# Kernel optimization log

Hardware: AMD Instinct MI355X
Metric: run time of the kernel (lower is better)

The kernel has to match this reference:

```python
import jax, jax.numpy as jnp
import numpy as np

N_NODES = 100000
N_EDGES = 1600000
F_IN = 128
HID = 128
N_CLS = 10
BN_EPS = 1e-5


def setup_inputs() -> dict:
    key = jax.random.key(0)
    ks = jax.random.split(key, 20)
    d = {}
    d['x'] = jax.random.normal(ks[0], (N_NODES, F_IN), dtype=jnp.float32)
    d['edge_index'] = jax.random.randint(ks[1], (2, N_EDGES), 0, N_NODES, dtype=jnp.int64)
    d['edge_weights'] = jax.random.uniform(ks[2], (N_EDGES,), dtype=jnp.float32)
    s1 = 1.0 / np.sqrt(F_IN)
    s2 = 1.0 / np.sqrt(HID)
    d['W1'] = jax.random.normal(ks[3], (F_IN, HID), dtype=jnp.float32) * s1
    d['b1'] = jax.random.normal(ks[4], (HID,), dtype=jnp.float32) * 0.01
    d['g1'] = jax.random.uniform(ks[5], (HID,), dtype=jnp.float32) + 0.5
    d['be1'] = jax.random.normal(ks[6], (HID,), dtype=jnp.float32) * 0.01
    d['W2'] = jax.random.normal(ks[7], (HID, HID), dtype=jnp.float32) * s2
    d['b2'] = jax.random.normal(ks[8], (HID,), dtype=jnp.float32) * 0.01
    d['g2'] = jax.random.uniform(ks[9], (HID,), dtype=jnp.float32) + 0.5
    d['be2'] = jax.random.normal(ks[10], (HID,), dtype=jnp.float32) * 0.01
    d['W3'] = jax.random.normal(ks[11], (HID, HID), dtype=jnp.float32) * s2
    d['b3'] = jax.random.normal(ks[12], (HID,), dtype=jnp.float32) * 0.01
    d['g3'] = jax.random.uniform(ks[13], (HID,), dtype=jnp.float32) + 0.5
    d['be3'] = jax.random.normal(ks[14], (HID,), dtype=jnp.float32) * 0.01
    d['Wlin'] = jax.random.normal(ks[15], (3 * HID, N_CLS), dtype=jnp.float32) / np.sqrt(3 * HID)
    d['blin'] = jax.random.normal(ks[16], (N_CLS,), dtype=jnp.float32) * 0.01
    return d


def _gcn_norm(edge_index, edge_weights, n):
    # add self loops with weight 1 (PyG gcn_norm default fill_value=1)
    loops = jnp.arange(n, dtype=edge_index.dtype)
    row = jnp.concatenate([edge_index[0], loops])   # source j
    col = jnp.concatenate([edge_index[1], loops])   # target i
    ew = jnp.concatenate([edge_weights, jnp.ones((n,), edge_weights.dtype)])
    deg = jax.ops.segment_sum(ew, col, num_segments=n)  # in-degree by weight
    dis = jnp.where(deg > 0, jax.lax.rsqrt(deg), 0.0)
    norm = dis[row] * ew * dis[col]                     # [E+N]
    return row, col, norm


def _gcn_conv(x, row, col, norm, W, b, n):
    h = x @ W                                            # [N, H]
    msg = h[row] * norm[:, None]                         # gather + scale
    out = jax.ops.segment_sum(msg, col, num_segments=n)  # scatter-add
    return out + b


def _bn_relu(x, g, be):
    # BatchNorm with track_running_stats=False: batch stats, biased variance
    mean = jnp.mean(x, axis=0)
    var = jnp.mean((x - mean) ** 2, axis=0)
    y = (x - mean) * jax.lax.rsqrt(var + BN_EPS) * g + be
    return jax.nn.relu(y)


def reference(x, edge_index, edge_weights, W1, b1, g1, be1, W2, b2, g2, be2,
              W3, b3, g3, be3, Wlin, blin):
    n = x.shape[0]
    row, col, norm = _gcn_norm(edge_index, edge_weights, n)
    o1 = _bn_relu(_gcn_conv(x, row, col, norm, W1, b1, n), g1, be1)
    o2 = _bn_relu(_gcn_conv(o1, row, col, norm, W2, b2, n), g2, be2)
    o3 = _bn_relu(_gcn_conv(o2, row, col, norm, W3, b3, n), g3, be3)
    emb = jnp.concatenate([o1, o2, o3], axis=1)          # [N, 3H]
    return emb @ Wlin + blin                             # [N, C]
```

## Files before the change

### kernel.cpp

```cpp
#include <hip/hip_runtime.h>

#define BN_EPS 1e-5f
#define AGG_GRID 2048
#define RED1 64
#define NB 512
#define CAP 4864
#define BIN_KE 16

typedef __attribute__((ext_vector_type(8))) short short8;
typedef __attribute__((ext_vector_type(4))) float f32x4;

static __device__ __forceinline__ float4 ld4(const float* p){ return *reinterpret_cast<const float4*>(p); }
static __device__ __forceinline__ void st4(float* p, float4 v){ *reinterpret_cast<float4*>(p) = v; }
static __device__ __forceinline__ unsigned short f2bf(float f){
  unsigned u = __float_as_uint(f);
  u += 0x7fffu + ((u>>16)&1u);
  return (unsigned short)(u>>16);
}
static __device__ __forceinline__ void fma_bf4(float4& a, float s, uint2 w){
  float v0 = __uint_as_float(w.x << 16);
  float v1 = __uint_as_float(w.x & 0xffff0000u);
  float v2 = __uint_as_float(w.y << 16);
  float v3 = __uint_as_float(w.y & 0xffff0000u);
  a.x = fmaf(s,v0,a.x); a.y = fmaf(s,v1,a.y); a.z = fmaf(s,v2,a.z); a.w = fmaf(s,v3,a.w);
}

__global__ __launch_bounds__(256) void k_zero(int* p, int n){
  int i = blockIdx.x*256 + threadIdx.x;
  if (i < n) p[i] = 0;
}

__global__ __launch_bounds__(256) void k_prepW(const float* __restrict__ W, unsigned short* __restrict__ Wt){
  int idx = blockIdx.x*256 + threadIdx.x;
  int k = idx >> 7, n = idx & 127;
  Wt[n*128 + k] = f2bf(W[idx]);
}

__global__ __launch_bounds__(256) void k_bin(const int* __restrict__ row, const int* __restrict__ col,
                                             const float* __restrict__ ew, int* __restrict__ bucketCnt,
                                             int2* __restrict__ bin, int E){
  __shared__ int hist[NB];
  int t = threadIdx.x;
  hist[t] = 0; hist[t+256] = 0;
  __syncthreads();
  int base0 = blockIdx.x*(256*BIN_KE) + t;
  int rank[BIN_KE];
  #pragma unroll
  for (int j=0;j<BIN_KE;++j){
    int e = base0 + j*256;
    if (e < E) rank[j] = atomicAdd(&hist[col[e]>>8], 1);
  }
  __syncthreads();
  int c0 = hist[t], c1 = hist[t+256];
  __syncthreads();
  if (c0) hist[t]     = atomicAdd(&bucketCnt[t],     c0);
  if (c1) hist[t+256] = atomicAdd(&bucketCnt[t+256], c1);
  __syncthreads();
  #pragma unroll
  for (int j=0;j<BIN_KE;++j){
    int e = base0 + j*256;
    if (e < E){
      int d = col[e];
      int bk = d >> 8;
      int pos = hist[bk] + rank[j];
      if (pos < CAP)
        bin[(size_t)bk*CAP + pos] = make_int2(row[e] | ((d & 255) << 17), __float_as_int(ew[e]));
    }
  }
}

__global__ void k_scan512(const int* __restrict__ cnt, int* __restrict__ start){
  __shared__ int sh[NB];
  int t = threadIdx.x;
  int c = cnt[t]; if (c > CAP) c = CAP;
  sh[t] = c;
  __syncthreads();
  for (int off=1; off<NB; off<<=1){
    int x = (t>=off) ? sh[t-off] : 0;
    __syncthreads();
    sh[t] += x;
    __syncthreads();
  }
  start[t] = sh[t] - c;
}

__global__ __launch_bounds__(256) void k_csr(const int2* __restrict__ bin, const int* __restrict__ bucketCnt,
                                             const int* __restrict__ bucketStart, int2* __restrict__ csr,
                                             int* __restrict__ rstart, float* __restrict__ deg, int N){
  __shared__ int hist[256], scn[256];
  __shared__ float degl[256];
  int b = blockIdx.x, t = threadIdx.x;
  hist[t] = 0; degl[t] = 0.f;
  __syncthreads();
  int m = bucketCnt[b]; if (m > CAP) m = CAP;
  const int2* bb = bin + (size_t)b*CAP;
  for (int i = t; i < m; i += 256){
    int2 r = bb[i];
    int dl = (r.x >> 17) & 255;
    atomicAdd(&hist[dl], 1);
    atomicAdd(&degl[dl], __int_as_float(r.y));
  }
  __syncthreads();
  int c = hist[t];
  scn[t] = c;
  __syncthreads();
  for (int off=1; off<256; off<<=1){
    int x = (t>=off) ? scn[t-off] : 0;
    __syncthreads();
    scn[t] += x;
    __syncthreads();
  }
  int base = bucketStart[b];
  int g = (b<<8) + t;
  if (g < N){
    rstart[g] = base + scn[t] - c;
    deg[g] = 1.f + degl[t];
    if (g == N-1) rstart[N] = base + scn[t];
  }
  __syncthreads();
  hist[t] = scn[t] - c;
  __syncthreads();
  for (int i = t; i < m; i += 256){
    int2 r = bb[i];
    int dl = (r.x >> 17) & 255;
    int pos = atomicAdd(&hist[dl], 1);
    csr[base + pos] = make_int2(r.x & 0x1FFFF, r.y);
  }
}

__global__ __launch_bounds__(256) void k_dis(const float* __restrict__ deg, float* __restrict__ dis, int N){
  int i = blockIdx.x*256 + threadIdx.x;
  if (i < N) dis[i] = rsqrtf(deg[i]);
}

__global__ __launch_bounds__(256) void k_norm(int2* __restrict__ csr, const float* __restrict__ dis, int M){
  int e = blockIdx.x*256 + threadIdx.x;
  if (e < M){
    int2 r = csr[e];
    r.y = __float_as_int(__int_as_float(r.y) * dis[r.x]);
    csr[e] = r;
  }
}

template<bool BN>
__global__ __launch_bounds__(256) void k_gemm_mfma(const float* __restrict__ A, const unsigned short* __restrict__ Wt,
                                                   const float* __restrict__ abv, unsigned short* __restrict__ h, int N){
  __shared__ unsigned short Al[64*136];
  __shared__ unsigned short Wl[128*136];
  int t = threadIdx.x;
  int row0 = blockIdx.x*64;
  #pragma unroll
  for (int i=0;i<8;++i){
    int idx = t + 256*i;
    int r = idx>>5, cg = idx&31;
    float4 v = make_float4(0.f,0.f,0.f,0.f);
    if (row0 + r < N) v = ld4(A + ((size_t)(row0+r)<<7) + cg*4);
    if (BN){
      float4 av = ld4(abv + cg*4), cv = ld4(abv + 128 + cg*4);
      v.x = fmaxf(fmaf(v.x,av.x,cv.x),0.f);
      v.y = fmaxf(fmaf(v.y,av.y,cv.y),0.f);
      v.z = fmaxf(fmaf(v.z,av.z,cv.z),0.f);
      v.w = fmaxf(fmaf(v.w,av.w,cv.w),0.f);
    }
    uint2 pk;
    pk.x = (unsigned)f2bf(v.x) | ((unsigned)f2bf(v.y)<<16);
    pk.y = (unsigned)f2bf(v.z) | ((unsigned)f2bf(v.w)<<16);
    *reinterpret_cast<uint2*>(&Al[r*136 + cg*4]) = pk;
  }
  #pragma unroll
  for (int i=0;i<8;++i){
    int idx = t + 256*i;
    int n = idx>>4, c8 = idx&15;
    *reinterpret_cast<uint4*>(&Wl[n*136 + c8*8]) =
      *reinterpret_cast<const uint4*>(&Wt[n*128 + c8*8]);
  }
  __syncthreads();

  int w = t>>6, lane = t&63, quad = lane>>4, lr = lane&15;
  f32x4 acc[8];
  #pragma unroll
  for (int j=0;j<8;++j) acc[j] = (f32x4){0.f,0.f,0.f,0.f};
  #pragma unroll
  for (int kk=0; kk<128; kk+=32){
    short8 a = *reinterpret_cast<const short8*>(&Al[(w*16+lr)*136 + kk + quad*8]);
    #pragma unroll
    for (int j=0;j<8;++j){
      short8 b = *reinterpret_cast<const short8*>(&Wl[(j*16+lr)*136 + kk + quad*8]);
      acc[j] = __builtin_amdgcn_mfma_f32_16x16x32_bf16(a, b, acc[j], 0, 0, 0);
    }
  }
  __syncthreads();
  #pragma unroll
  for (int j=0;j<8;++j)
    #pragma unroll
    for (int r=0;r<4;++r)
      Al[(w*16 + quad*4 + r)*136 + j*16 + lr] = f2bf(acc[j][r]);
  __syncthreads();
  #pragma unroll
  for (int i=0;i<8;++i){
    int idx = t + 256*i;
    int r = idx>>5, cg = idx&31;
    if (row0 + r < N)
      *reinterpret_cast<uint2*>(&h[((size_t)(row0+r)<<7) + cg*4]) =
        *reinterpret_cast<const uint2*>(&Al[r*136 + cg*4]);
  }
}

__global__ __launch_bounds__(256) void k_agg(const unsigned short* __restrict__ h, const int2* __restrict__ csr,
                                             const int* __restrict__ rstart, const float* __restrict__ dis,
                                             const float* __restrict__ bias, float* __restrict__ o,
                                             float* __restrict__ partials, int N){
  __shared__ float ls[256];
  int t = threadIdx.x;
  ls[t] = 0.f;
  __syncthreads();
  int lane = t & 31, gy = t >> 5;
  float4 bv = ld4(bias + lane*4);
  float4 ssum = make_float4(0.f,0.f,0.f,0.f);
  float4 ssq  = make_float4(0.f,0.f,0.f,0.f);
  for (int g = blockIdx.x*8 + gy; g < N; g += AGG_GRID*8){
    int s = rstart[g], n = rstart[g+1] - s;
    float dg = dis[g];
    float4 acc = make_float4(0.f,0.f,0.f,0.f);
    fma_bf4(acc, dg*dg, *reinterpret_cast<const uint2*>(h + ((size_t)g<<7) + lane*4));
    int i = 0;
    for (; i+3 < n; i += 4){
      int2 s0 = csr[s+i], s1 = csr[s+i+1], s2 = csr[s+i+2], s3 = csr[s+i+3];
      uint2 r0 = *reinterpret_cast<const uint2*>(h + ((size_t)s0.x<<7) + lane*4);
      uint2 r1 = *reinterpret_cast<const uint2*>(h + ((size_t)s1.x<<7) + lane*4);
      uint2 r2 = *reinterpret_cast<const uint2*>(h + ((size_t)s2.x<<7) + lane*4);
      uint2 r3 = *reinterpret_cast<const uint2*>(h + ((size_t)s3.x<<7) + lane*4);
      fma_bf4(acc, __int_as_float(s0.y)*dg, r0);
      fma_bf4(acc, __int_as_float(s1.y)*dg, r1);
      fma_bf4(acc, __int_as_float(s2.y)*dg, r2);
      fma_bf4(acc, __int_as_float(s3.y)*dg, r3);
    }
    for (; i < n; ++i){
      int2 s0 = csr[s+i];
      fma_bf4(acc, __int_as_float(s0.y)*dg, *reinterpret_cast<const uint2*>(h + ((size_t)s0.x<<7) + lane*4));
    }
    acc.x += bv.x; acc.y += bv.y; acc.z += bv.z; acc.w += bv.w;
    st4(o + ((size_t)g<<7) + lane*4, acc);
    ssum.x += acc.x; ssum.y += acc.y; ssum.z += acc.z; ssum.w += acc.w;
    ssq.x = fmaf(acc.x,acc.x,ssq.x); ssq.y = fmaf(acc.y,acc.y,ssq.y);
    ssq.z = fmaf(acc.z,acc.z,ssq.z); ssq.w = fmaf(acc.w,acc.w,ssq.w);
  }
  int f = lane*4;
  atomicAdd(&ls[f+0], ssum.x); atomicAdd(&ls[f+1], ssum.y);
  atomicAdd(&ls[f+2], ssum.z); atomicAdd(&ls[f+3], ssum.w);
  atomicAdd(&ls[128+f+0], ssq.x); atomicAdd(&ls[128+f+1], ssq.y);
  atomicAdd(&ls[128+f+2], ssq.z); atomicAdd(&ls[128+f+3], ssq.w);
  __syncthreads();
  partials[(size_t)blockIdx.x*256 + t] = ls[t];
}

__global__ __launch_bounds__(256) void k_bn_red1(const float* __restrict__ partials, float* __restrict__ out1){
  int t = threadIdx.x, b = blockIdx.x;
  int rows = AGG_GRID / RED1;
  const float* p = partials + (size_t)b*rows*256;
  float s0 = 0.f, s1 = 0.f, s2 = 0.f, s3 = 0.f;
  for (int i=0;i<rows;i+=4){
    s0 += p[(size_t)(i+0)*256 + t];
    s1 += p[(size_t)(i+1)*256 + t];
    s2 += p[(size_t)(i+2)*256 + t];
    s3 += p[(size_t)(i+3)*256 + t];
  }
  out1[(size_t)b*256 + t] = (s0+s1)+(s2+s3);
}

__global__ void k_bn_fin(const float* __restrict__ out1, const float* __restrict__ gam,
                         const float* __restrict__ bet, float* __restrict__ ab, int N){
  __shared__ float sh[256];
  int t = threadIdx.x;
  float s = 0.f;
  #pragma unroll 4
  for (int i=0;i<RED1;++i) s += out1[(size_t)i*256 + t];
  sh[t] = s;
  __syncthreads();
  if (t < 128){
    float invN = 1.f/(float)N;
    float mean = sh[t]*invN;
    float var = fmaxf(sh[128+t]*invN - mean*mean, 0.f);
    float a = gam[t]*rsqrtf(var + BN_EPS);
    ab[t] = a;
    ab[128+t] = bet[t] - mean*a;
  }
}

__global__ __launch_bounds__(256) void k_lin(const float* __restrict__ o, const float* __restrict__ Wl_g,
                                             const float* __restrict__ blin, const float* __restrict__ ab,
                                             float* __restrict__ out, int N, int initFlag){
  __shared__ float Wl[1280];
  __shared__ float abL[256];
  int t = threadIdx.x;
  for (int i=t;i<1280;i+=256) Wl[i] = Wl_g[i];
  abL[t] = ab[t];
  __syncthreads();
  int row = blockIdx.x*256 + t;
  if (row >= N) return;
  float acc[10];
  #pragma unroll
  for (int c=0;c<10;++c) acc[c] = initFlag ? blin[c] : out[(size_t)row*10 + c];
  const float* orow = o + ((size_t)row<<7);
  #pragma unroll 4
  for (int k=0;k<128;k+=4){
    float4 v = ld4(orow + k);
    float4 av = ld4(abL + k), cv = ld4(abL + 128 + k);
    v.x = fmaxf(fmaf(v.x,av.x,cv.x),0.f);
    v.y = fmaxf(fmaf(v.y,av.y,cv.y),0.f);
    v.z = fmaxf(fmaf(v.z,av.z,cv.z),0.f);
    v.w = fmaxf(fmaf(v.w,av.w,cv.w),0.f);
    #pragma unroll
    for (int c=0;c<10;++c){
      acc[c] = fmaf(v.x, Wl[(k+0)*10+c], acc[c]);
      acc[c] = fmaf(v.y, Wl[(k+1)*10+c], acc[c]);
      acc[c] = fmaf(v.z, Wl[(k+2)*10+c], acc[c]);
      acc[c] = fmaf(v.w, Wl[(k+3)*10+c], acc[c]);
    }
  }
  #pragma unroll
  for (int c=0;c<10;++c) out[(size_t)row*10 + c] = acc[c];
}


extern "C" void kernel_launch(void* const* d_in, const int* in_sizes, int n_in,
                              void* d_out, int out_size, void* d_ws, size_t ws_size,
                              hipStream_t stream){
  const float* x    = (const float*)d_in[0];
  const int*   ei   = (const int*)d_in[1];
  const float* ew   = (const float*)d_in[2];
  const float* W[3]  = {(const float*)d_in[3], (const float*)d_in[7],  (const float*)d_in[11]};
  const float* b[3]  = {(const float*)d_in[4], (const float*)d_in[8],  (const float*)d_in[12]};
  const float* g[3]  = {(const float*)d_in[5], (const float*)d_in[9],  (const float*)d_in[13]};
  const float* be[3] = {(const float*)d_in[6], (const float*)d_in[10], (const float*)d_in[14]};
  const float* Wlin = (const float*)d_in[15];
  const float* blin = (const float*)d_in[16];
  float* out = (float*)d_out;

  int N = in_sizes[0] / 128;
  int E = in_sizes[2];
  const int* row = ei;
  const int* col = ei + E;

  char* p = (char*)d_ws;
  auto carve = [&](size_t bytes) -> void* {
    void* q = (void*)p;
    p += (bytes + 255) & ~(size_t)255;
    return q;
  };
  int*   bucketCnt   = (int*)  carve((size_t)NB*4);
  int*   bucketStart = (int*)  carve((size_t)NB*4);
  float* deg      = (float*)carve((size_t)N*4);
  float* dis      = (float*)carve((size_t)N*4);
  int*   rstart   = (int*)  carve((size_t)(N+1)*4);
  float* partials = (float*)carve((size_t)AGG_GRID*256*4);
  float* red1     = (float*)carve((size_t)RED1*256*4);
  float* ab       = (float*)carve(3*256*4);
  unsigned short* Wt = (unsigned short*)carve((size_t)3*128*128*2);
  unsigned short* h  = (unsigned short*)carve((size_t)N*128*2);
  float* o        = (float*)carve((size_t)N*512);
  int2*  csr      = (int2*) carve((size_t)E*8);
  int2*  bin      = (int2*) carve((size_t)NB*CAP*8);

  int gN = (N+255)/256, gE = (E+255)/256;
  int gBin = (E + 256*BIN_KE - 1) / (256*BIN_KE);

  k_zero<<<2,256,0,stream>>>(bucketCnt, NB);
  for (int l=0;l<3;++l)
    k_prepW<<<64,256,0,stream>>>(W[l], Wt + (size_t)l*128*128);
  k_bin    <<<gBin,256,0,stream>>>(row, col, ew, bucketCnt, bin, E);
  k_scan512<<<1,NB,0,stream>>>(bucketCnt, bucketStart);
  k_csr    <<<NB,256,0,stream>>>(bin, bucketCnt, bucketStart, csr, rstart, deg, N);
  k_dis    <<<gN,256,0,stream>>>(deg, dis, N);
  k_norm   <<<gE,256,0,stream>>>(csr, dis, E);

  int gGemm = (N+63)/64;
  for (int l=0;l<3;++l){
    float* abl = ab + l*256;
    const unsigned short* Wtl = Wt + (size_t)l*128*128;
    if (l == 0) k_gemm_mfma<false><<<gGemm,256,0,stream>>>(x, Wtl, nullptr, h, N);
    else        k_gemm_mfma<true> <<<gGemm,256,0,stream>>>(o, Wtl, ab + (l-1)*256, h, N);
    k_agg    <<<AGG_GRID,256,0,stream>>>(h, csr, rstart, dis, b[l], o, partials, N);
    k_bn_red1<<<RED1,256,0,stream>>>(partials, red1);
    k_bn_fin <<<1,256,0,stream>>>(red1, g[l], be[l], abl, N);
    k_lin    <<<gN,256,0,stream>>>(o, Wlin + (size_t)l*1280, blin, abl, out, N, l==0 ? 1 : 0);
  }
}
```

Measured before the change: 556.6 us.

## Fuse final linear into next-layer GEMM via MFMA and store activations as bf16

The per-layer classifier projection for layers 1 and 2 is folded into the following layer's MFMA GEMM as an extra 16-wide output tile, using a pre-transposed bf16 Wlin, so two separate k_lin passes over the activations go away. The aggregation output o is now stored as bf16 instead of fp32, halving its write and re-read traffic in the GEMM and the last k_lin. The aggregation inner loop also gets an 8-way unrolled gather. BN statistics are still taken from the fp32 values before rounding, but the stored activations and the projection inputs lose precision to bf16.

Measured after the change: 556.7 us. No clear change (+0.0%).

```diff
diff --git a/kernel.cpp b/kernel.cpp
--- a/kernel.cpp
+++ b/kernel.cpp
@@ -24,6 +24,16 @@
   float v3 = __uint_as_float(w.y & 0xffff0000u);
   a.x = fmaf(s,v0,a.x); a.y = fmaf(s,v1,a.y); a.z = fmaf(s,v2,a.z); a.w = fmaf(s,v3,a.w);
 }
+static __device__ __forceinline__ float4 unpack_bf4(uint2 w){
+  return make_float4(__uint_as_float(w.x << 16), __uint_as_float(w.x & 0xffff0000u),
+                     __uint_as_float(w.y << 16), __uint_as_float(w.y & 0xffff0000u));
+}
+static __device__ __forceinline__ uint2 pack_bf4(float4 v){
+  uint2 pk;
+  pk.x = (unsigned)f2bf(v.x) | ((unsigned)f2bf(v.y)<<16);
+  pk.y = (unsigned)f2bf(v.z) | ((unsigned)f2bf(v.w)<<16);
+  return pk;
+}
 
 __global__ __launch_bounds__(256) void k_zero(int* p, int n){
   int i = blockIdx.x*256 + threadIdx.x;
@@ -34,6 +44,15 @@
   int idx = blockIdx.x*256 + threadIdx.x;
   int k = idx >> 7, n = idx & 127;
   Wt[n*128 + k] = f2bf(W[idx]);
+}
+
+__global__ __launch_bounds__(256) void k_prepWlin(const float* __restrict__ Wlin, unsigned short* __restrict__ WlinT){
+  int idx = blockIdx.x*256 + threadIdx.x;
+  if (idx >= 6144) return;
+  int l = idx >> 11, rem = idx & 2047;
+  int n = rem >> 7, k = rem & 127;
+  float v = (n < 10) ? Wlin[((size_t)l*128 + k)*10 + n] : 0.f;
+  WlinT[(size_t)l*2048 + n*128 + k] = f2bf(v);
 }
 
 __global__ __launch_bounds__(256) void k_bin(const int* __restrict__ row, const int* __restrict__ col,
@@ -142,9 +161,11 @@
   }
 }
 
-template<bool BN>
-__global__ __launch_bounds__(256) void k_gemm_mfma(const float* __restrict__ A, const unsigned short* __restrict__ Wt,
-                                                   const float* __restrict__ abv, unsigned short* __restrict__ h, int N){
+template<bool BN, bool LIN, bool LININIT>
+__global__ __launch_bounds__(256) void k_gemm_mfma(const void* __restrict__ Ap, const unsigned short* __restrict__ Wt,
+                                                   const float* __restrict__ abv, unsigned short* __restrict__ h,
+                                                   const unsigned short* __restrict__ WlinT,
+                                                   const float* __restrict__ blin, float* __restrict__ out, int N){
   __shared__ unsigned short Al[64*136];
   __shared__ unsigned short Wl[128*136];
   int t = threadIdx.x;
@@ -153,19 +174,21 @@
   for (int i=0;i<8;++i){
     int idx = t + 256*i;
     int r = idx>>5, cg = idx&31;
-    float4 v = make_float4(0.f,0.f,0.f,0.f);
-    if (row0 + r < N) v = ld4(A + ((size_t)(row0+r)<<7) + cg*4);
-    if (BN){
+    float4 v;
+    if (!BN){
+      v = make_float4(0.f,0.f,0.f,0.f);
+      if (row0 + r < N) v = ld4((const float*)Ap + ((size_t)(row0+r)<<7) + cg*4);
+    } else {
+      uint2 raw = make_uint2(0u,0u);
+      if (row0 + r < N) raw = *reinterpret_cast<const uint2*>((const unsigned short*)Ap + ((size_t)(row0+r)<<7) + cg*4);
+      v = unpack_bf4(raw);
       float4 av = ld4(abv + cg*4), cv = ld4(abv + 128 + cg*4);
       v.x = fmaxf(fmaf(v.x,av.x,cv.x),0.f);
       v.y = fmaxf(fmaf(v.y,av.y,cv.y),0.f);
       v.z = fmaxf(fmaf(v.z,av.z,cv.z),0.f);
       v.w = fmaxf(fmaf(v.w,av.w,cv.w),0.f);
     }
-    uint2 pk;
-    pk.x = (unsigned)f2bf(v.x) | ((unsigned)f2bf(v.y)<<16);
-    pk.y = (unsigned)f2bf(v.z) | ((unsigned)f2bf(v.w)<<16);
-    *reinterpret_cast<uint2*>(&Al[r*136 + cg*4]) = pk;
+    *reinterpret_cast<uint2*>(&Al[r*136 + cg*4]) = pack_bf4(v);
   }
   #pragma unroll
   for (int i=0;i<8;++i){
@@ -174,12 +197,20 @@
     *reinterpret_cast<uint4*>(&Wl[n*136 + c8*8]) =
       *reinterpret_cast<const uint4*>(&Wt[n*128 + c8*8]);
   }
-  __syncthreads();
 
   int w = t>>6, lane = t&63, quad = lane>>4, lr = lane&15;
+  short8 bl[4];
+  if (LIN){
+    #pragma unroll
+    for (int q4=0;q4<4;++q4)
+      bl[q4] = *reinterpret_cast<const short8*>(&WlinT[lr*128 + q4*32 + quad*8]);
+  }
+  __syncthreads();
+
   f32x4 acc[8];
   #pragma unroll
   for (int j=0;j<8;++j) acc[j] = (f32x4){0.f,0.f,0.f,0.f};
+  f32x4 accL = (f32x4){0.f,0.f,0.f,0.f};
   #pragma unroll
   for (int kk=0; kk<128; kk+=32){
     short8 a = *reinterpret_cast<const short8*>(&Al[(w*16+lr)*136 + kk + quad*8]);
@@ -188,6 +219,17 @@
       short8 b = *reinterpret_cast<const short8*>(&Wl[(j*16+lr)*136 + kk + quad*8]);
       acc[j] = __builtin_amdgcn_mfma_f32_16x16x32_bf16(a, b, acc[j], 0, 0, 0);
     }
+    if (LIN) accL = __builtin_amdgcn_mfma_f32_16x16x32_bf16(a, bl[kk>>5], accL, 0, 0, 0);
+  }
+  if (LIN && lr < 10){
+    #pragma unroll
+    for (int r=0;r<4;++r){
+      int rr = row0 + w*16 + quad*4 + r;
+      if (rr < N){
+        if (LININIT) out[(size_t)rr*10 + lr] = blin[lr] + accL[r];
+        else         out[(size_t)rr*10 + lr] += accL[r];
+      }
+    }
   }
   __syncthreads();
   #pragma unroll
@@ -208,7 +250,7 @@
 
 __global__ __launch_bounds__(256) void k_agg(const unsigned short* __restrict__ h, const int2* __restrict__ csr,
                                              const int* __restrict__ rstart, const float* __restrict__ dis,
-                                             const float* __restrict__ bias, float* __restrict__ o,
+                                             const float* __restrict__ bias, unsigned short* __restrict__ o,
                                              float* __restrict__ partials, int N){
   __shared__ float ls[256];
   int t = threadIdx.x;
@@ -224,23 +266,43 @@
     float4 acc = make_float4(0.f,0.f,0.f,0.f);
     fma_bf4(acc, dg*dg, *reinterpret_cast<const uint2*>(h + ((size_t)g<<7) + lane*4));
     int i = 0;
+    for (; i+7 < n; i += 8){
+      int2 e0 = csr[s+i],   e1 = csr[s+i+1], e2 = csr[s+i+2], e3 = csr[s+i+3];
+      int2 e4 = csr[s+i+4], e5 = csr[s+i+5], e6 = csr[s+i+6], e7 = csr[s+i+7];
+      uint2 r0 = *reinterpret_cast<const uint2*>(h + ((size_t)e0.x<<7) + lane*4);
+      uint2 r1 = *reinterpret_cast<const uint2*>(h + ((size_t)e1.x<<7) + lane*4);
+      uint2 r2 = *reinterpret_cast<const uint2*>(h + ((size_t)e2.x<<7) + lane*4);
+      uint2 r3 = *reinterpret_cast<const uint2*>(h + ((size_t)e3.x<<7) + lane*4);
+      uint2 r4 = *reinterpret_cast<const uint2*>(h + ((size_t)e4.x<<7) + lane*4);
+      uint2 r5 = *reinterpret_cast<const uint2*>(h + ((size_t)e5.x<<7) + lane*4);
+      uint2 r6 = *reinterpret_cast<const uint2*>(h + ((size_t)e6.x<<7) + lane*4);
+      uint2 r7 = *reinterpret_cast<const uint2*>(h + ((size_t)e7.x<<7) + lane*4);
+      fma_bf4(acc, __int_as_float(e0.y)*dg, r0);
+      fma_bf4(acc, __int_as_float(e1.y)*dg, r1);
+      fma_bf4(acc, __int_as_float(e2.y)*dg, r2);
+      fma_bf4(acc, __int_as_float(e3.y)*dg, r3);
+      fma_bf4(acc, __int_as_float(e4.y)*dg, r4);
+      fma_bf4(acc, __int_as_float(e5.y)*dg, r5);
+      fma_bf4(acc, __int_as_float(e6.y)*dg, r6);
+      fma_bf4(acc, __int_as_float(e7.y)*dg, r7);
+    }
     for (; i+3 < n; i += 4){
-      int2 s0 = csr[s+i], s1 = csr[s+i+1], s2 = csr[s+i+2], s3 = csr[s+i+3];
-      uint2 r0 = *reinterpret_cast<const uint2*>(h + ((size_t)s0.x<<7) + lane*4);
-      uint2 r1 = *reinterpret_cast<const uint2*>(h + ((size_t)s1.x<<7) + lane*4);
-      uint2 r2 = *reinterpret_cast<const uint2*>(h + ((size_t)s2.x<<7) + lane*4);
-      uint2 r3 = *reinterpret_cast<const uint2*>(h + ((size_t)s3.x<<7) + lane*4);
-      fma_bf4(acc, __int_as_float(s0.y)*dg, r0);
-      fma_bf4(acc, __int_as_float(s1.y)*dg, r1);
-      fma_bf4(acc, __int_as_float(s2.y)*dg, r2);
-      fma_bf4(acc, __int_as_float(s3.y)*dg, r3);
+      int2 e0 = csr[s+i], e1 = csr[s+i+1], e2 = csr[s+i+2], e3 = csr[s+i+3];
+      uint2 r0 = *reinterpret_cast<const uint2*>(h + ((size_t)e0.x<<7) + lane*4);
+      uint2 r1 = *reinterpret_cast<const uint2*>(h + ((size_t)e1.x<<7) + lane*4);
+      uint2 r2 = *reinterpret_cast<const uint2*>(h + ((size_t)e2.x<<7) + lane*4);
+      uint2 r3 = *reinterpret_cast<const uint2*>(h + ((size_t)e3.x<<7) + lane*4);
+      fma_bf4(acc, __int_as_float(e0.y)*dg, r0);
+      fma_bf4(acc, __int_as_float(e1.y)*dg, r1);
+      fma_bf4(acc, __int_as_float(e2.y)*dg, r2);
+      fma_bf4(acc, __int_as_float(e3.y)*dg, r3);
     }
     for (; i < n; ++i){
-      int2 s0 = csr[s+i];
-      fma_bf4(acc, __int_as_float(s0.y)*dg, *reinterpret_cast<const uint2*>(h + ((size_t)s0.x<<7) + lane*4));
+      int2 e0 = csr[s+i];
+      fma_bf4(acc, __int_as_float(e0.y)*dg, *reinterpret_cast<const uint2*>(h + ((size_t)e0.x<<7) + lane*4));
     }
     acc.x += bv.x; acc.y += bv.y; acc.z += bv.z; acc.w += bv.w;
-    st4(o + ((size_t)g<<7) + lane*4, acc);
+    *reinterpret_cast<uint2*>(o + ((size_t)g<<7) + lane*4) = pack_bf4(acc);
     ssum.x += acc.x; ssum.y += acc.y; ssum.z += acc.z; ssum.w += acc.w;
     ssq.x = fmaf(acc.x,acc.x,ssq.x); ssq.y = fmaf(acc.y,acc.y,ssq.y);
     ssq.z = fmaf(acc.z,acc.z,ssq.z); ssq.w = fmaf(acc.w,acc.w,ssq.w);
@@ -287,9 +349,8 @@
   }
 }
 
-__global__ __launch_bounds__(256) void k_lin(const float* __restrict__ o, const float* __restrict__ Wl_g,
-                                             const float* __restrict__ blin, const float* __restrict__ ab,
-                                             float* __restrict__ out, int N, int initFlag){
+__global__ __launch_bounds__(256) void k_lin(const unsigned short* __restrict__ o, const float* __restrict__ Wl_g,
+                                             const float* __restrict__ ab, float* __restrict__ out, int N){
   __shared__ float Wl[1280];
   __shared__ float abL[256];
   int t = threadIdx.x;
@@ -300,11 +361,11 @@
   if (row >= N) return;
   float acc[10];
   #pragma unroll
-  for (int c=0;c<10;++c) acc[c] = initFlag ? blin[c] : out[(size_t)row*10 + c];
-  const float* orow = o + ((size_t)row<<7);
+  for (int c=0;c<10;++c) acc[c] = out[(size_t)row*10 + c];
+  const unsigned short* orow = o + ((size_t)row<<7);
   #pragma unroll 4
   for (int k=0;k<128;k+=4){
-    float4 v = ld4(orow + k);
+    float4 v = unpack_bf4(*reinterpret_cast<const uint2*>(orow + k));
     float4 av = ld4(abL + k), cv = ld4(abL + 128 + k);
     v.x = fmaxf(fmaf(v.x,av.x,cv.x),0.f);
     v.y = fmaxf(fmaf(v.y,av.y,cv.y),0.f);
@@ -356,9 +417,10 @@
   float* partials = (float*)carve((size_t)AGG_GRID*256*4);
   float* red1     = (float*)carve((size_t)RED1*256*4);
   float* ab       = (float*)carve(3*256*4);
-  unsigned short* Wt = (unsigned short*)carve((size_t)3*128*128*2);
+  unsigned short* Wt    = (unsigned short*)carve((size_t)3*128*128*2);
+  unsigned short* WlinT = (unsigned short*)carve((size_t)3*16*128*2);
   unsigned short* h  = (unsigned short*)carve((size_t)N*128*2);
-  float* o        = (float*)carve((size_t)N*512);
+  unsigned short* o  = (unsigned short*)carve((size_t)N*128*2);
   int2*  csr      = (int2*) carve((size_t)E*8);
   int2*  bin      = (int2*) carve((size_t)NB*CAP*8);
 
@@ -368,6 +430,7 @@
   k_zero<<<2,256,0,stream>>>(bucketCnt, NB);
   for (int l=0;l<3;++l)
     k_prepW<<<64,256,0,stream>>>(W[l], Wt + (size_t)l*128*128);
+  k_prepWlin<<<24,256,0,stream>>>(Wlin, WlinT);
   k_bin    <<<gBin,256,0,stream>>>(row, col, ew, bucketCnt, bin, E);
   k_scan512<<<1,NB,0,stream>>>(bucketCnt, bucketStart);
   k_csr    <<<NB,256,0,stream>>>(bin, bucketCnt, bucketStart, csr, rstart, deg, N);
@@ -375,14 +438,17 @@
   k_norm   <<<gE,256,0,stream>>>(csr, dis, E);
 
   int gGemm = (N+63)/64;
-  for (int l=0;l<3;++l){
-    float* abl = ab + l*256;
-    const unsigned short* Wtl = Wt + (size_t)l*128*128;
-    if (l == 0) k_gemm_mfma<false><<<gGemm,256,0,stream>>>(x, Wtl, nullptr, h, N);
-    else        k_gemm_mfma<true> <<<gGemm,256,0,stream>>>(o, Wtl, ab + (l-1)*256, h, N);
-    k_agg    <<<AGG_GRID,256,0,stream>>>(h, csr, rstart, dis, b[l], o, partials, N);
-    k_bn_red1<<<RED1,256,0,stream>>>(partials, red1);
-    k_bn_fin <<<1,256,0,stream>>>(red1, g[l], be[l], abl, N);
-    k_lin    <<<gN,256,0,stream>>>(o, Wlin + (size_t)l*1280, blin, abl, out, N, l==0 ? 1 : 0);
-  }
-}
+  k_gemm_mfma<false,false,false><<<gGemm,256,0,stream>>>(x, Wt, nullptr, h, nullptr, nullptr, nullptr, N);
+  k_agg    <<<AGG_GRID,256,0,stream>>>(h, csr, rstart, dis, b[0], o, partials, N);
+  k_bn_red1<<<RED1,256,0,stream>>>(partials, red1);
+  k_bn_fin <<<1,256,0,stream>>>(red1, g[0], be[0], ab, N);
+  k_gemm_mfma<true,true,true><<<gGemm,256,0,stream>>>(o, Wt + 128*128, ab, h, WlinT, blin, out, N);
+  k_agg    <<<AGG_GRID,256,0,stream>>>(h, csr, rstart, dis, b[1], o, partials, N);
+  k_bn_red1<<<RED1,256,0,stream>>>(partials, red1);
+  k_bn_fin <<<1,256,0,stream>>>(red1, g[1], be[1], ab + 256, N);
+  k_gemm_mfma<true,true,false><<<gGemm,256,0,stream>>>(o, Wt + 2*128*128, ab + 256, h, WlinT + 2048, blin, out, N);
+  k_agg    <<<AGG_GRID,256,0,stream>>>(h, csr, rstart, dis, b[2], o, partials, N);
+  k_bn_red1<<<RED1,256,0,stream>>>(partials, red1);
+  k_bn_fin <<<1,256,0,stream>>>(red1, g[2], be[2], ab + 512, N);
+  k_lin    <<<gN,256,0,stream>>>(o, Wlin + (size_t)2*1280, ab + 512, out, N);
+}
```
